# Optimization experiments

Measured on AMD Instinct MI355X. Metric: run time of the kernel, lower is better.

The kernel has to match this reference:

```python
import jax, jax.numpy as jnp
import numpy as np

B, F, D, L, N = 2048, 40, 64, 3, 40  # batch, num_fields, embed_dim, num_layers, num_subspaces


def setup_inputs() -> dict:
    key = jax.random.key(0)
    inputs = jax.random.normal(key, (B, F, D), dtype=jnp.float32)
    # Parameters per layer, matching torch init exactly:
    #   W     = identity(D) repeated over out_subspaces -> [N, D, D]
    #   alpha = ones([num_fields, in_subspaces, out_subspaces]); in_subspaces == F for
    #           layer 0 and == N afterwards; with N == F all layers share shape [F, N, N]
    #   h     = ones([N, D, 1])
    W = jnp.broadcast_to(jnp.eye(D, dtype=jnp.float32), (L, N, D, D)).copy()
    alpha = jnp.ones((L, F, N, N), dtype=jnp.float32)
    h = jnp.ones((L, N, D, 1), dtype=jnp.float32)
    return {"inputs": inputs, "W": W, "alpha": alpha, "h": h}


def _fusion_layer(B0, Bi, W, alpha, h):
    # Original math: fusion[b,n,D,d] = sum_{f,i} alpha[f,i,n] * B0[b,f,D] * Bi[b,i,d]
    #                out[b,n,D]     = sum_d fusion[b,n,D,d] * W[n,D,d] * h[n,d]
    # Reordered to avoid the [b,f,n,D,d] outer-product tensor:
    M = W * h[:, :, 0][:, None, :]                 # [n, D, d] = W * h broadcast over D
    C = jnp.einsum('bid,nDd->binD', Bi, M)         # contract embed dim d first
    out = jnp.einsum('bfD,fin,binD->bnD', B0, alpha, C)
    return out


def reference(inputs, W, alpha, h):
    B_i = inputs
    for l in range(L):
        B_i = _fusion_layer(inputs, B_i, W[l], alpha[l], h[l])
    return B_i
```

## Files before the change

### kernel.cpp

```cpp
#include <hip/hip_runtime.h>


typedef __bf16 bf16x8 __attribute__((ext_vector_type(8)));
typedef float  f32x16 __attribute__((ext_vector_type(16)));
typedef unsigned short us4 __attribute__((ext_vector_type(4)));

constexpr int BATCH = 2048;
constexpr int FDIM  = 40;
constexpr int DDIM  = 64;
constexpr int LAY   = 3;
constexpr int FPAD  = 48;
constexpr int APAD  = 56;
constexpr int NSPL  = 4;
constexpr int NPB   = FDIM / NSPL;
constexpr int BPB   = 8;
constexpr int MSLAB = DDIM * DDIM;
constexpr int ASLAB = DDIM * APAD;

__device__ __forceinline__ unsigned short f2bf(float f) {
  union { float f; unsigned u; } v; v.f = f;
  unsigned r = v.u + 0x7fff + ((v.u >> 16) & 1);
  return (unsigned short)(r >> 16);
}

__device__ __forceinline__ void dma16(unsigned short* lds, const unsigned short* g) {
  __builtin_amdgcn_global_load_lds(
      (const __attribute__((address_space(1))) unsigned int*)g,
      (__attribute__((address_space(3))) unsigned int*)lds, 16, 0, 0);
}

__global__ __launch_bounds__(256) void prep_all(
    const float* __restrict__ inputs, const float* __restrict__ W,
    const float* __restrict__ h, const float* __restrict__ alpha,
    unsigned short* __restrict__ B0b, unsigned short* __restrict__ B0T,
    unsigned short* __restrict__ M, unsigned short* __restrict__ AT) {
  __shared__ float lds[FDIM][DDIM + 1];
  if (blockIdx.x < BATCH) {
    const int b = blockIdx.x;
    const float* src = inputs + (size_t)b * FDIM * DDIM;
    for (int cch = threadIdx.x; cch < FDIM * DDIM / 4; cch += 256) {
      float4 v = reinterpret_cast<const float4*>(src)[cch];
      int e = cch * 4;
      int f = e >> 6, d = e & 63;
      lds[f][d] = v.x; lds[f][d + 1] = v.y; lds[f][d + 2] = v.z; lds[f][d + 3] = v.w;
      us4 o = { f2bf(v.x), f2bf(v.y), f2bf(v.z), f2bf(v.w) };
      reinterpret_cast<us4*>(B0b + (size_t)b * FDIM * DDIM)[cch] = o;
    }
    __syncthreads();
    for (int cch = threadIdx.x; cch < DDIM * FPAD / 4; cch += 256) {
      int f4 = cch % (FPAD / 4);
      int d  = cch / (FPAD / 4);
      us4 o = {0, 0, 0, 0};
      if (f4 < FDIM / 4) {
        int f = f4 * 4;
        o[0] = f2bf(lds[f][d]);     o[1] = f2bf(lds[f + 1][d]);
        o[2] = f2bf(lds[f + 2][d]); o[3] = f2bf(lds[f + 3][d]);
      }
      reinterpret_cast<us4*>(B0T + (size_t)b * DDIM * FPAD)[cch] = o;
    }
    return;
  }
  int j = (blockIdx.x - BATCH) * 256 + threadIdx.x;
  const int nM4  = LAY * FDIM * MSLAB / 4;
  const int nAl4 = LAY * FDIM * FDIM * FDIM / 4;
  if (j < nM4) {
    int e   = j * 4;
    int ln  = e >> 12;
    int row = (e >> 6) & 63;
    int jc  = (e >> 3) & 7;
    int o   = e & 7;
    int ds  = ((jc ^ (row & 7)) << 3) + o;
    float4 wv = *reinterpret_cast<const float4*>(W + ((size_t)ln * 64 + row) * 64 + ds);
    float4 hv = *reinterpret_cast<const float4*>(h + (size_t)ln * 64 + ds);
    us4 ov = { f2bf(wv.x * hv.x), f2bf(wv.y * hv.y), f2bf(wv.z * hv.z), f2bf(wv.w * hv.w) };
    *reinterpret_cast<us4*>(M + e) = ov;
    return;
  }
  j -= nM4;
  if (j >= nAl4) return;
  {
    int e = j * 4;
    int n = e % FDIM;
    int i = (e / FDIM) % FDIM;
    int f = (e / (FDIM * FDIM)) % FDIM;
    int l = e / (FDIM * FDIM * FDIM);
    float4 v = *reinterpret_cast<const float4*>(alpha + e);
    unsigned short* dst = AT + ((size_t)l * FDIM) * ASLAB + (size_t)i * APAD + f;
#pragma unroll
    for (int k = 0; k < 4; ++k) {
      float vk = (k == 0) ? v.x : (k == 1) ? v.y : (k == 2) ? v.z : v.w;
      dst[(size_t)(n + k) * ASLAB] = f2bf(vk);
    }
  }
}

template <bool FINAL>
__global__ __launch_bounds__(256, 2) void layer_k(
    const unsigned short* __restrict__ Bi,
    const unsigned short* __restrict__ B0T,
    const unsigned short* __restrict__ Mt,
    const unsigned short* __restrict__ ATt,
    void* __restrict__ outp)
{
  __shared__ unsigned short smM[2][MSLAB];
  __shared__ unsigned short smA[2][ASLAB];

  const int tid  = threadIdx.x;
  const int lane = tid & 63;
  const int w    = tid >> 6;
  const int c    = lane & 31;
  const int h    = lane >> 5;

  const int L  = (blockIdx.x & 7) * 128 + (blockIdx.x >> 3);
  const int bg = L >> 2;
  const int ns = L & 3;
  const int nBase = ns * NPB;
  const int bb = bg * BPB + w * 2;

  bf16x8 aBi[2][2][4];
#pragma unroll
  for (int b2 = 0; b2 < 2; ++b2)
#pragma unroll
    for (int it = 0; it < 2; ++it) {
      int row = it * 32 + c; if (row > FDIM - 1) row = FDIM - 1;
#pragma unroll
      for (int ks = 0; ks < 4; ++ks)
        aBi[b2][it][ks] = *reinterpret_cast<const bf16x8*>(
            Bi + ((size_t)(bb + b2) * FDIM + row) * DDIM + ks * 16 + h * 8);
    }
  bf16x8 bT[2][2][3];
#pragma unroll
  for (int b2 = 0; b2 < 2; ++b2)
#pragma unroll
    for (int dt = 0; dt < 2; ++dt)
#pragma unroll
      for (int ks = 0; ks < 3; ++ks)
        bT[b2][dt][ks] = *reinterpret_cast<const bf16x8*>(
            B0T + ((size_t)(bb + b2) * DDIM + dt * 32 + c) * FPAD + ks * 16 + h * 8);

  auto dmaChunk = [&](int nl, int bs) {
    const unsigned short* Ms = Mt  + (size_t)(nBase + nl) * MSLAB;
    const unsigned short* As = ATt + (size_t)(nBase + nl) * ASLAB;
#pragma unroll
    for (int r = 0; r < 2; ++r) {
      int k = tid + r * 256;
      dma16(&smM[bs][k * 8], Ms + k * 8);
    }
    dma16(&smA[bs][tid * 8], As + tid * 8);
    if (tid < 192) dma16(&smA[bs][(tid + 256) * 8], As + (tid + 256) * 8);
  };

  auto compute = [&](int nl, int bs) {
    const int n = nBase + nl;
    const unsigned short* mL = &smM[bs][0];
    const unsigned short* aL = &smA[bs][0];
    bf16x8 mb[2][4], at[2][3];
#pragma unroll
    for (int dt = 0; dt < 2; ++dt)
#pragma unroll
      for (int ks = 0; ks < 4; ++ks)
        mb[dt][ks] = *reinterpret_cast<const bf16x8*>(
            mL + (dt * 32 + c) * 64 + (((ks * 2 + h) ^ (c & 7)) * 8));
#pragma unroll
    for (int it = 0; it < 2; ++it)
#pragma unroll
      for (int ks = 0; ks < 3; ++ks)
        at[it][ks] = *reinterpret_cast<const bf16x8*>(
            aL + (it * 32 + c) * APAD + (ks * 2 + h) * 8);

    float pout[2][2] = {{0.f, 0.f}, {0.f, 0.f}};

    f32x16 cA, rA, cB, rB;

    auto issueT = [&](int b2, int dt, int it, f32x16& cc, f32x16& rr) {
      f32x16 c0 = {0,0,0,0,0,0,0,0,0,0,0,0,0,0,0,0};
      f32x16 r0 = {0,0,0,0,0,0,0,0,0,0,0,0,0,0,0,0};
#pragma unroll
      for (int ks = 0; ks < 3; ++ks) {
        c0 = __builtin_amdgcn_mfma_f32_32x32x16_bf16(aBi[b2][it][ks], mb[dt][ks], c0, 0, 0, 0);
        r0 = __builtin_amdgcn_mfma_f32_32x32x16_bf16(at[it][ks], bT[b2][dt][ks], r0, 0, 0, 0);
      }
      cc = __builtin_amdgcn_mfma_f32_32x32x16_bf16(aBi[b2][it][3], mb[dt][3], c0, 0, 0, 0);
      rr = r0;
    };
    auto combineT = [&](int b2, int dt, const f32x16& cc, const f32x16& rr) {
      float t0 = 0.f, t1 = 0.f, t2 = 0.f, t3 = 0.f;
#pragma unroll
      for (int r = 0; r < 4; ++r) {
        t0 += cc[r] * rr[r];         t1 += cc[r + 4] * rr[r + 4];
        t2 += cc[r + 8] * rr[r + 8]; t3 += cc[r + 12] * rr[r + 12];
      }
      pout[b2][dt] += (t0 + t1) + (t2 + t3);
    };

    issueT(0, 0, 0, cA, rA);
    issueT(1, 0, 0, cB, rB); combineT(0, 0, cA, rA);
    issueT(0, 1, 0, cA, rA); combineT(1, 0, cB, rB);
    issueT(1, 1, 0, cB, rB); combineT(0, 1, cA, rA);
    issueT(0, 0, 1, cA, rA); combineT(1, 1, cB, rB);
    issueT(1, 0, 1, cB, rB); combineT(0, 0, cA, rA);
    issueT(0, 1, 1, cA, rA); combineT(1, 0, cB, rB);
    issueT(1, 1, 1, cB, rB); combineT(0, 1, cA, rA);
    combineT(1, 1, cB, rB);

#pragma unroll
    for (int b2 = 0; b2 < 2; ++b2) {
      float v0 = pout[b2][0] + __shfl_xor(pout[b2][0], 32, 64);
      float v1 = pout[b2][1] + __shfl_xor(pout[b2][1], 32, 64);
      float val = h ? v1 : v0;
      size_t off = ((size_t)(bb + b2) * FDIM + n) * DDIM + lane;
      if (FINAL) ((float*)outp)[off] = val;
      else       ((unsigned short*)outp)[off] = f2bf(val);
    }
  };

  dmaChunk(0, 0);
  __syncthreads();
#pragma unroll 1
  for (int cc = 0; cc < NPB; ++cc) {
    const int bs = cc & 1;
    if (cc + 1 < NPB) dmaChunk(cc + 1, bs ^ 1);
    compute(cc, bs);
    __syncthreads();
  }
}

extern "C" void kernel_launch(void* const* d_in, const int* in_sizes, int n_in,
                              void* d_out, int out_size, void* d_ws, size_t ws_size,
                              hipStream_t stream) {
  const float* inputs = (const float*)d_in[0];
  const float* W      = (const float*)d_in[1];
  const float* alpha  = (const float*)d_in[2];
  const float* h      = (const float*)d_in[3];

  char* ws = (char*)d_ws;
  const size_t S   = (size_t)BATCH * FDIM * DDIM * 2;
  const size_t ST  = (size_t)BATCH * DDIM * FPAD * 2;
  unsigned short* Bi1 = (unsigned short*)(ws);
  unsigned short* Bi2 = (unsigned short*)(ws + S);
  unsigned short* B0b = (unsigned short*)(ws + 2 * S);
  unsigned short* B0T = (unsigned short*)(ws + 3 * S);
  unsigned short* Mb  = (unsigned short*)(ws + 3 * S + ST);
  unsigned short* ATb = (unsigned short*)(ws + 3 * S + ST + (size_t)LAY * FDIM * MSLAB * 2);

  hipMemsetAsync(ATb, 0, (size_t)LAY * FDIM * ASLAB * 2, stream);

  const int nPrep4 = (LAY * FDIM * MSLAB + LAY * FDIM * FDIM * FDIM) / 4;
  const int prepBlocks = BATCH + (nPrep4 + 255) / 256;
  prep_all<<<prepBlocks, 256, 0, stream>>>(inputs, W, h, alpha, B0b, B0T, Mb, ATb);

  dim3 grid(BATCH / BPB * NSPL), blk(256);
  const size_t mL = (size_t)FDIM * MSLAB;
  const size_t aL = (size_t)FDIM * ASLAB;
  layer_k<false><<<grid, blk, 0, stream>>>(B0b, B0T, Mb, ATb, Bi1);
  layer_k<false><<<grid, blk, 0, stream>>>(Bi1, B0T, Mb + mL, ATb + aL, Bi2);
  layer_k<true ><<<grid, blk, 0, stream>>>(Bi2, B0T, Mb + 2 * mL, ATb + 2 * aL, d_out);
}
```

Before: 241.9 us.

## Assign one batch per wave and raise occupancy to three blocks per CU

Each wave now handles a single batch element instead of two, which halves the register-resident Bi/B0T fragments and the accumulators. Launch bounds go from 2 to 3 blocks per CU, and the block index mapping is adjusted for twice as many blocks. The hand-interleaved MFMA/combine schedule is replaced by a plain loop. The cost is that each LDS chunk of M and alpha is now reused across half as many batches, so DMA traffic per unit of compute doubles, and the explicit overlap of MFMA issue with the combine step is lost.

```diff
diff --git a/kernel.cpp b/kernel.cpp
--- a/kernel.cpp
+++ b/kernel.cpp
@@ -13,7 +13,7 @@
 constexpr int APAD  = 56;
 constexpr int NSPL  = 4;
 constexpr int NPB   = FDIM / NSPL;
-constexpr int BPB   = 8;
+constexpr int BPB   = 4;
 constexpr int MSLAB = DDIM * DDIM;
 constexpr int ASLAB = DDIM * APAD;
 
@@ -95,7 +95,7 @@
 }
 
 template <bool FINAL>
-__global__ __launch_bounds__(256, 2) void layer_k(
+__global__ __launch_bounds__(256, 3) void layer_k(
     const unsigned short* __restrict__ Bi,
     const unsigned short* __restrict__ B0T,
     const unsigned short* __restrict__ Mt,
@@ -111,32 +111,28 @@
   const int c    = lane & 31;
   const int h    = lane >> 5;
 
-  const int L  = (blockIdx.x & 7) * 128 + (blockIdx.x >> 3);
+  const int L  = (blockIdx.x & 7) * 256 + (blockIdx.x >> 3);
   const int bg = L >> 2;
   const int ns = L & 3;
   const int nBase = ns * NPB;
-  const int bb = bg * BPB + w * 2;
-
-  bf16x8 aBi[2][2][4];
-#pragma unroll
-  for (int b2 = 0; b2 < 2; ++b2)
-#pragma unroll
-    for (int it = 0; it < 2; ++it) {
-      int row = it * 32 + c; if (row > FDIM - 1) row = FDIM - 1;
-#pragma unroll
-      for (int ks = 0; ks < 4; ++ks)
-        aBi[b2][it][ks] = *reinterpret_cast<const bf16x8*>(
-            Bi + ((size_t)(bb + b2) * FDIM + row) * DDIM + ks * 16 + h * 8);
-    }
-  bf16x8 bT[2][2][3];
-#pragma unroll
-  for (int b2 = 0; b2 < 2; ++b2)
-#pragma unroll
-    for (int dt = 0; dt < 2; ++dt)
-#pragma unroll
-      for (int ks = 0; ks < 3; ++ks)
-        bT[b2][dt][ks] = *reinterpret_cast<const bf16x8*>(
-            B0T + ((size_t)(bb + b2) * DDIM + dt * 32 + c) * FPAD + ks * 16 + h * 8);
+  const int b  = bg * BPB + w;
+
+  bf16x8 aBi[2][4];
+#pragma unroll
+  for (int it = 0; it < 2; ++it) {
+    int row = it * 32 + c; if (row > FDIM - 1) row = FDIM - 1;
+#pragma unroll
+    for (int ks = 0; ks < 4; ++ks)
+      aBi[it][ks] = *reinterpret_cast<const bf16x8*>(
+          Bi + ((size_t)b * FDIM + row) * DDIM + ks * 16 + h * 8);
+  }
+  bf16x8 bT[2][3];
+#pragma unroll
+  for (int dt = 0; dt < 2; ++dt)
+#pragma unroll
+    for (int ks = 0; ks < 3; ++ks)
+      bT[dt][ks] = *reinterpret_cast<const bf16x8*>(
+          B0T + ((size_t)b * DDIM + dt * 32 + c) * FPAD + ks * 16 + h * 8);
 
   auto dmaChunk = [&](int nl, int bs) {
     const unsigned short* Ms = Mt  + (size_t)(nBase + nl) * MSLAB;
@@ -168,50 +164,35 @@
         at[it][ks] = *reinterpret_cast<const bf16x8*>(
             aL + (it * 32 + c) * APAD + (ks * 2 + h) * 8);
 
-    float pout[2][2] = {{0.f, 0.f}, {0.f, 0.f}};
-
-    f32x16 cA, rA, cB, rB;
-
-    auto issueT = [&](int b2, int dt, int it, f32x16& cc, f32x16& rr) {
-      f32x16 c0 = {0,0,0,0,0,0,0,0,0,0,0,0,0,0,0,0};
-      f32x16 r0 = {0,0,0,0,0,0,0,0,0,0,0,0,0,0,0,0};
-#pragma unroll
-      for (int ks = 0; ks < 3; ++ks) {
-        c0 = __builtin_amdgcn_mfma_f32_32x32x16_bf16(aBi[b2][it][ks], mb[dt][ks], c0, 0, 0, 0);
-        r0 = __builtin_amdgcn_mfma_f32_32x32x16_bf16(at[it][ks], bT[b2][dt][ks], r0, 0, 0, 0);
+    float pout[2] = {0.f, 0.f};
+#pragma unroll
+    for (int it = 0; it < 2; ++it) {
+#pragma unroll
+      for (int dt = 0; dt < 2; ++dt) {
+        f32x16 cc = {0,0,0,0,0,0,0,0,0,0,0,0,0,0,0,0};
+        f32x16 rr = {0,0,0,0,0,0,0,0,0,0,0,0,0,0,0,0};
+#pragma unroll
+        for (int ks = 0; ks < 3; ++ks) {
+          cc = __builtin_amdgcn_mfma_f32_32x32x16_bf16(aBi[it][ks], mb[dt][ks], cc, 0, 0, 0);
+          rr = __builtin_amdgcn_mfma_f32_32x32x16_bf16(at[it][ks], bT[dt][ks], rr, 0, 0, 0);
+        }
+        cc = __builtin_amdgcn_mfma_f32_32x32x16_bf16(aBi[it][3], mb[dt][3], cc, 0, 0, 0);
+        float t0 = 0.f, t1 = 0.f, t2 = 0.f, t3 = 0.f;
+#pragma unroll
+        for (int r = 0; r < 4; ++r) {
+          t0 += cc[r] * rr[r];         t1 += cc[r + 4] * rr[r + 4];
+          t2 += cc[r + 8] * rr[r + 8]; t3 += cc[r + 12] * rr[r + 12];
+        }
+        pout[dt] += (t0 + t1) + (t2 + t3);
       }
-      cc = __builtin_amdgcn_mfma_f32_32x32x16_bf16(aBi[b2][it][3], mb[dt][3], c0, 0, 0, 0);
-      rr = r0;
-    };
-    auto combineT = [&](int b2, int dt, const f32x16& cc, const f32x16& rr) {
-      float t0 = 0.f, t1 = 0.f, t2 = 0.f, t3 = 0.f;
-#pragma unroll
-      for (int r = 0; r < 4; ++r) {
-        t0 += cc[r] * rr[r];         t1 += cc[r + 4] * rr[r + 4];
-        t2 += cc[r + 8] * rr[r + 8]; t3 += cc[r + 12] * rr[r + 12];
-      }
-      pout[b2][dt] += (t0 + t1) + (t2 + t3);
-    };
-
-    issueT(0, 0, 0, cA, rA);
-    issueT(1, 0, 0, cB, rB); combineT(0, 0, cA, rA);
-    issueT(0, 1, 0, cA, rA); combineT(1, 0, cB, rB);
-    issueT(1, 1, 0, cB, rB); combineT(0, 1, cA, rA);
-    issueT(0, 0, 1, cA, rA); combineT(1, 1, cB, rB);
-    issueT(1, 0, 1, cB, rB); combineT(0, 0, cA, rA);
-    issueT(0, 1, 1, cA, rA); combineT(1, 0, cB, rB);
-    issueT(1, 1, 1, cB, rB); combineT(0, 1, cA, rA);
-    combineT(1, 1, cB, rB);
-
-#pragma unroll
-    for (int b2 = 0; b2 < 2; ++b2) {
-      float v0 = pout[b2][0] + __shfl_xor(pout[b2][0], 32, 64);
-      float v1 = pout[b2][1] + __shfl_xor(pout[b2][1], 32, 64);
-      float val = h ? v1 : v0;
-      size_t off = ((size_t)(bb + b2) * FDIM + n) * DDIM + lane;
-      if (FINAL) ((float*)outp)[off] = val;
-      else       ((unsigned short*)outp)[off] = f2bf(val);
-    }
+    }
+
+    float v0 = pout[0] + __shfl_xor(pout[0], 32, 64);
+    float v1 = pout[1] + __shfl_xor(pout[1], 32, 64);
+    float val = h ? v1 : v0;
+    size_t off = ((size_t)b * FDIM + n) * DDIM + lane;
+    if (FINAL) ((float*)outp)[off] = val;
+    else       ((unsigned short*)outp)[off] = f2bf(val);
   };
 
   dmaChunk(0, 0);
```

New measurement: 564.9 us. 2.34x slower.
